# Performance work log

Measured on AMD Instinct MI355X. Metric: run time of the kernel, lower is better.

Reference implementation:

```python
import math
import jax, jax.numpy as jnp
import numpy as np

HIDDEN = 1024
HEADS = 16
HEAD_DIM = 64
THETA = 10000.0
TRAIN_LEN = 2048
SCALE = 4.0
ALPHA = 1.0
BETA = 32.0
B, T = 2, 2048


def _yarn_inv_freq_and_mscale():
    """YaRN (NTK-by-parts) inverse frequencies + attention mscale."""
    half = HEAD_DIM // 2
    pos_freqs = THETA ** (jnp.arange(half, dtype=jnp.float32) * 2.0 / HEAD_DIM)
    inv_freq_extra = 1.0 / pos_freqs              # extrapolation (original RoPE)
    inv_freq_inter = 1.0 / (SCALE * pos_freqs)    # interpolation (position scaling)

    def find_dim(num_rot):
        return (HEAD_DIM * math.log(TRAIN_LEN / (num_rot * 2.0 * math.pi))) / (2.0 * math.log(THETA))

    low = max(math.floor(find_dim(BETA)), 0)
    high = min(math.ceil(find_dim(ALPHA)), half - 1)
    ramp = jnp.clip((jnp.arange(half, dtype=jnp.float32) - low) / max(high - low, 1e-3), 0.0, 1.0)
    extrap_factor = 1.0 - ramp  # 1 -> pure extrapolation (high-freq dims)
    inv_freq = inv_freq_inter * (1.0 - extrap_factor) + inv_freq_extra * extrap_factor
    mscale = 0.1 * math.log(SCALE) + 1.0 if SCALE > 1.0 else 1.0
    return inv_freq, mscale


def _rotate_half(x):
    h = x.shape[-1] // 2
    return jnp.concatenate([-x[..., h:], x[..., :h]], axis=-1)


def _apply_rope(q, k, position_ids):
    inv_freq, mscale = _yarn_inv_freq_and_mscale()
    # angles: (B, L, T, HEAD_DIM//2)
    angles = position_ids.astype(jnp.float32)[..., None] * inv_freq
    cos = jnp.concatenate([jnp.cos(angles)] * 2, axis=-1).astype(q.dtype)
    sin = jnp.concatenate([jnp.sin(angles)] * 2, axis=-1).astype(q.dtype)
    q_rot = q * cos + _rotate_half(q) * sin
    k_rot = k * cos + _rotate_half(k) * sin
    return q_rot, k_rot, mscale


def setup_inputs() -> dict:
    key = jax.random.key(0)
    ks = jax.random.split(key, 7)
    packed_embeddings = jax.random.normal(ks[0], (B, HEADS, T, HIDDEN), dtype=jnp.float32)
    position_ids = jnp.sort(jax.random.randint(ks[1], (B, HEADS, T), 0, T), axis=-1).astype(jnp.int32)
    active_mask = jax.random.randint(ks[2], (B, HEADS, T), 0, 2).astype(jnp.bool_)
    # Xavier-uniform per-head projection params
    lim_in = math.sqrt(6.0 / (HIDDEN + HEAD_DIM))
    q_proj = jax.random.uniform(ks[3], (HEADS, HIDDEN, HEAD_DIM), minval=-lim_in, maxval=lim_in, dtype=jnp.float32)
    k_proj = jax.random.uniform(ks[4], (HEADS, HIDDEN, HEAD_DIM), minval=-lim_in, maxval=lim_in, dtype=jnp.float32)
    v_proj = jax.random.uniform(ks[5], (HEADS, HIDDEN, HEAD_DIM), minval=-lim_in, maxval=lim_in, dtype=jnp.float32)
    o_proj = jax.random.uniform(ks[6], (HEADS, HEAD_DIM, HIDDEN), minval=-lim_in, maxval=lim_in, dtype=jnp.float32)
    return {"packed_embeddings": packed_embeddings, "position_ids": position_ids,
            "active_mask": active_mask, "q_proj": q_proj, "k_proj": k_proj,
            "v_proj": v_proj, "o_proj": o_proj}


def reference(packed_embeddings, position_ids, active_mask, q_proj, k_proj, v_proj, o_proj):
    # per-head projections: (B,L,T,d) x (L,d,u) -> (B,L,T,u)
    q = jnp.einsum('bltd,ldu->bltu', packed_embeddings, q_proj)
    k = jnp.einsum('bltd,ldu->bltu', packed_embeddings, k_proj)
    v = jnp.einsum('bltd,ldu->bltu', packed_embeddings, v_proj)
    q, k, mscale = _apply_rope(q, k, position_ids)

    # cache=None path: num_tokens_processed = 0, key mask = active mask, key_len = T
    scale = mscale / math.sqrt(HEAD_DIM)
    scores = jnp.einsum('bltu,blsu->blts', q, k) * scale  # (B,L,T,T)
    causal = jnp.tril(jnp.ones((T, T), dtype=jnp.bool_))
    mask = active_mask[:, :, :, None] & active_mask[:, :, None, :] & causal
    neg = jnp.finfo(scores.dtype).min
    probs = jax.nn.softmax(jnp.where(mask, scores, neg), axis=-1)
    attended = jnp.einsum('blts,blsu->bltu', probs, v)
    # zero fully-masked (inactive) query rows, matching flex_attention skipping them
    attended = attended * active_mask[..., None].astype(attended.dtype)
    return jnp.einsum('bltu,lud->bltd', attended, o_proj)
```

## Files before the change

kernel.cpp:

```cpp
#include <hip/hip_runtime.h>
#include <hip/hip_bf16.h>
#include <math.h>

typedef __attribute__((ext_vector_type(8))) short bf16x8;
typedef __attribute__((ext_vector_type(4))) float f32x4;

static constexpr int Bn = 2, Ln = 16, Tn = 2048, Dn = 1024, Un = 64;
static constexpr float SCALE_ATTN = 0.14232867951f;
static constexpr int VTS = 2080;

__device__ __forceinline__ unsigned short f2bf(float x) {
    __hip_bfloat16 h = __float2bfloat16(x);
    return *reinterpret_cast<unsigned short*>(&h);
}
__device__ __forceinline__ unsigned int pk2(float a, float b) {
    return (unsigned int)f2bf(a) | ((unsigned int)f2bf(b) << 16);
}
__device__ __forceinline__ float inv_freq_of(int d) {
    float p = powf(10000.0f, (float)d * (1.0f / 32.0f));
    float ramp = fminf(fmaxf(((float)d - 8.0f) * (1.0f / 13.0f), 0.0f), 1.0f);
    return (0.25f / p) * ramp + (1.0f / p) * (1.0f - ramp);
}

__global__ __launch_bounds__(256) void prep_w(
    const float* __restrict__ qp, const float* __restrict__ kp,
    const float* __restrict__ vp, const float* __restrict__ op,
    unsigned short* __restrict__ qt, unsigned short* __restrict__ kt,
    unsigned short* __restrict__ vt, unsigned short* __restrict__ ot)
{
    __shared__ unsigned short T[64][72];
    const int m = blockIdx.z, l = blockIdx.y, x = blockIdx.x;
    const int tid = (int)threadIdx.x;
    const float* sb = (m == 0 ? qp : m == 1 ? kp : m == 2 ? vp : op) + (size_t)l * 65536;
    unsigned short* db = (m == 0 ? qt : m == 1 ? kt : m == 2 ? vt : ot) + (size_t)l * 65536;
    #pragma unroll
    for (int p = 0; p < 4; ++p) {
        int r = (tid >> 4) + 16 * p, c4 = (tid & 15) * 4;
        size_t s = (m < 3) ? ((size_t)(64 * x + r) * 64 + c4)
                           : ((size_t)r * 1024 + 64 * x + c4);
        float4 v = *(const float4*)(sb + s);
        T[r][c4 + 0] = f2bf(v.x); T[r][c4 + 1] = f2bf(v.y);
        T[r][c4 + 2] = f2bf(v.z); T[r][c4 + 3] = f2bf(v.w);
    }
    __syncthreads();
    #pragma unroll
    for (int p = 0; p < 2; ++p) {
        int task = tid + 256 * p;
        int c = task >> 3, g = task & 7;
        uint4 wv; unsigned short* wp = (unsigned short*)&wv;
        #pragma unroll
        for (int j = 0; j < 8; ++j) wp[j] = T[8 * g + j][c];
        size_t d = (m < 3) ? ((size_t)c * 1024 + 64 * x + 8 * g)
                           : ((size_t)(64 * x + c) * 64 + 8 * g);
        *(uint4*)(db + d) = wv;
    }
}

__global__ __launch_bounds__(256) void qkv_rope(
    const float* __restrict__ emb, const int* __restrict__ pos,
    const unsigned short* __restrict__ qt, const unsigned short* __restrict__ kt,
    const unsigned short* __restrict__ vt,
    unsigned short* __restrict__ Qw, unsigned short* __restrict__ Kw,
    unsigned short* __restrict__ Vt)
{
    __shared__ unsigned short A_lds[64][40];
    __shared__ unsigned short O_lds[64][200];
    const int z = blockIdx.y, l = z & 15, row0 = blockIdx.x * 64;
    const int tid = (int)threadIdx.x;
    const int w = tid >> 6, lane = tid & 63, hi = lane >> 4, lo = lane & 15;

    f32x4 acc[12];
    #pragma unroll
    for (int i = 0; i < 12; ++i) acc[i] = (f32x4){0.f, 0.f, 0.f, 0.f};

    const float* embB = emb + ((size_t)z * Tn + row0) * Dn;
    const unsigned short* wq = qt + (size_t)l * 65536;
    const unsigned short* wk = kt + (size_t)l * 65536;
    const unsigned short* wv = vt + (size_t)l * 65536;

    for (int k0 = 0; k0 < Dn; k0 += 32) {
        {
            int r = tid >> 2, c8 = (tid & 3) * 8;
            const float* s = embB + (size_t)r * Dn + k0 + c8;
            float4 v0 = *(const float4*)s, v1 = *(const float4*)(s + 4);
            uint4 u = {pk2(v0.x, v0.y), pk2(v0.z, v0.w), pk2(v1.x, v1.y), pk2(v1.z, v1.w)};
            *(uint4*)&A_lds[r][c8] = u;
        }
        __syncthreads();
        bf16x8 a = *(const bf16x8*)&A_lds[16 * w + lo][8 * hi];
        #pragma unroll
        for (int n = 0; n < 12; ++n) {
            const unsigned short* wb = (n < 4) ? wq : (n < 8) ? wk : wv;
            const unsigned short* bp = wb + (size_t)(16 * (n & 3) + lo) * 1024 + k0 + 8 * hi;
            bf16x8 b = *(const bf16x8*)bp;
            acc[n] = __builtin_amdgcn_mfma_f32_16x16x32_bf16(a, b, acc[n], 0, 0, 0);
        }
        __syncthreads();
    }

    const float if0 = inv_freq_of(lo);
    const float if1 = inv_freq_of(16 + lo);
    #pragma unroll
    for (int r = 0; r < 4; ++r) {
        int orow = 16 * w + 4 * hi + r;
        float fp = (float)pos[(size_t)z * Tn + row0 + orow];
        float s0, c0, s1, c1;
        sincosf(fp * if0, &s0, &c0);
        sincosf(fp * if1, &s1, &c1);
        float qa = acc[0][r], qb = acc[2][r], qc = acc[1][r], qd = acc[3][r];
        O_lds[orow][lo]           = f2bf(qa * c0 - qb * s0);
        O_lds[orow][lo + 32]      = f2bf(qb * c0 + qa * s0);
        O_lds[orow][16 + lo]      = f2bf(qc * c1 - qd * s1);
        O_lds[orow][16 + lo + 32] = f2bf(qd * c1 + qc * s1);
        float ka = acc[4][r], kb = acc[6][r], kc = acc[5][r], kd = acc[7][r];
        O_lds[orow][64 + lo]      = f2bf(ka * c0 - kb * s0);
        O_lds[orow][64 + lo + 32] = f2bf(kb * c0 + ka * s0);
        O_lds[orow][80 + lo]      = f2bf(kc * c1 - kd * s1);
        O_lds[orow][80 + lo + 32] = f2bf(kd * c1 + kc * s1);
        O_lds[orow][128 + lo]     = f2bf(acc[8][r]);
        O_lds[orow][144 + lo]     = f2bf(acc[9][r]);
        O_lds[orow][160 + lo]     = f2bf(acc[10][r]);
        O_lds[orow][176 + lo]     = f2bf(acc[11][r]);
    }
    __syncthreads();
    #pragma unroll
    for (int p = 0; p < 2; ++p) {
        int task = tid + 256 * p, t = task >> 3, g = task & 7;
        *(uint4*)(Qw + ((size_t)z * Tn + row0 + t) * 64 + 8 * g) = *(uint4*)&O_lds[t][8 * g];
        *(uint4*)(Kw + ((size_t)z * Tn + row0 + t) * 64 + 8 * g) = *(uint4*)&O_lds[t][64 + 8 * g];
    }
    #pragma unroll
    for (int p = 0; p < 2; ++p) {
        int task = tid + 256 * p, d = task & 63, g = task >> 6;
        uint4 wv4; unsigned short* wp = (unsigned short*)&wv4;
        #pragma unroll
        for (int j = 0; j < 8; ++j) wp[j] = O_lds[8 * g + j][128 + d];
        *(uint4*)(Vt + (size_t)z * 64 * VTS + (size_t)d * VTS + row0 + 8 * g) = wv4;
    }
}

__global__ __launch_bounds__(256) void flash_attn(
    const unsigned short* __restrict__ Qw, const unsigned short* __restrict__ Kw,
    const unsigned short* __restrict__ Vt, const int* __restrict__ act,
    unsigned short* __restrict__ At)
{
    __shared__ unsigned short K_lds[64][72];
    __shared__ unsigned short V_lds[64][72];
    __shared__ unsigned short P_lds[64][72];
    __shared__ unsigned char aK[64];
    const int z = blockIdx.y;
    const int rt = (int)gridDim.x - 1 - (int)blockIdx.x;
    const int row0 = rt * 64;
    const int tid = (int)threadIdx.x;
    const int w = tid >> 6, lane = tid & 63, hi = lane >> 4, lo = lane & 15;

    const unsigned short* qb = Qw + ((size_t)z * Tn + row0 + 16 * w + lo) * 64 + 8 * hi;
    bf16x8 aq0 = *(const bf16x8*)qb;
    bf16x8 aq1 = *(const bf16x8*)(qb + 32);

    bool aqv[4]; float m_[4], ls[4];
    f32x4 accO[4];
    #pragma unroll
    for (int r = 0; r < 4; ++r) {
        aqv[r] = act[(size_t)z * Tn + row0 + 16 * w + 4 * hi + r] != 0;
        m_[r] = -INFINITY; ls[r] = 0.f;
        accO[r] = (f32x4){0.f, 0.f, 0.f, 0.f};
    }

    for (int kt = 0; kt <= rt; ++kt) {
        const int j0 = kt * 64;
        __syncthreads();
        {
            int r = tid >> 2, c = tid & 3;
            const unsigned short* s = Kw + ((size_t)z * Tn + j0 + r) * 64 + 16 * c;
            *(uint4*)&K_lds[r][16 * c]     = *(const uint4*)s;
            *(uint4*)&K_lds[r][16 * c + 8] = *(const uint4*)(s + 8);
            const unsigned short* v = Vt + (size_t)z * 64 * VTS + (size_t)r * VTS + j0 + 16 * c;
            *(uint4*)&V_lds[r][16 * c]     = *(const uint4*)v;
            *(uint4*)&V_lds[r][16 * c + 8] = *(const uint4*)(v + 8);
        }
        if (tid < 64) aK[tid] = (unsigned char)(act[(size_t)z * Tn + j0 + tid] != 0);
        __syncthreads();

        f32x4 s4[4];
        #pragma unroll
        for (int n = 0; n < 4; ++n) s4[n] = (f32x4){0.f, 0.f, 0.f, 0.f};
        #pragma unroll
        for (int n = 0; n < 4; ++n) {
            bf16x8 b0 = *(const bf16x8*)&K_lds[16 * n + lo][8 * hi];
            bf16x8 b1 = *(const bf16x8*)&K_lds[16 * n + lo][32 + 8 * hi];
            s4[n] = __builtin_amdgcn_mfma_f32_16x16x32_bf16(aq0, b0, s4[n], 0, 0, 0);
            s4[n] = __builtin_amdgcn_mfma_f32_16x16x32_bf16(aq1, b1, s4[n], 0, 0, 0);
        }
        unsigned char akn[4];
        #pragma unroll
        for (int n = 0; n < 4; ++n) akn[n] = aK[16 * n + lo];

        #pragma unroll
        for (int r = 0; r < 4; ++r) {
            const int rowg = row0 + 16 * w + 4 * hi + r;
            float sv[4];
            #pragma unroll
            for (int n = 0; n < 4; ++n) {
                int col = j0 + 16 * n + lo;
                sv[n] = (aqv[r] && akn[n] && col <= rowg) ? s4[n][r] * SCALE_ATTN : -INFINITY;
            }
            float mt = fmaxf(fmaxf(sv[0], sv[1]), fmaxf(sv[2], sv[3]));
            mt = fmaxf(mt, __shfl_xor(mt, 1));
            mt = fmaxf(mt, __shfl_xor(mt, 2));
            mt = fmaxf(mt, __shfl_xor(mt, 4));
            mt = fmaxf(mt, __shfl_xor(mt, 8));
            float mnew = fmaxf(m_[r], mt);
            float p[4], corr;
            if (mnew == -INFINITY) {
                p[0] = p[1] = p[2] = p[3] = 0.f; corr = 1.f;
            } else {
                corr = __expf(m_[r] - mnew);
                #pragma unroll
                for (int n = 0; n < 4; ++n) p[n] = __expf(sv[n] - mnew);
            }
            float ps = p[0] + p[1] + p[2] + p[3];
            ps += __shfl_xor(ps, 1);
            ps += __shfl_xor(ps, 2);
            ps += __shfl_xor(ps, 4);
            ps += __shfl_xor(ps, 8);
            m_[r] = mnew;
            ls[r] = ls[r] * corr + ps;
            #pragma unroll
            for (int n2 = 0; n2 < 4; ++n2) accO[n2][r] *= corr;
            int prow = 16 * w + 4 * hi + r;
            P_lds[prow][lo]      = f2bf(p[0]);
            P_lds[prow][16 + lo] = f2bf(p[1]);
            P_lds[prow][32 + lo] = f2bf(p[2]);
            P_lds[prow][48 + lo] = f2bf(p[3]);
        }
        __syncthreads();

        bf16x8 ap0 = *(const bf16x8*)&P_lds[16 * w + lo][8 * hi];
        bf16x8 ap1 = *(const bf16x8*)&P_lds[16 * w + lo][32 + 8 * hi];
        #pragma unroll
        for (int n2 = 0; n2 < 4; ++n2) {
            bf16x8 b0 = *(const bf16x8*)&V_lds[16 * n2 + lo][8 * hi];
            bf16x8 b1 = *(const bf16x8*)&V_lds[16 * n2 + lo][32 + 8 * hi];
            accO[n2] = __builtin_amdgcn_mfma_f32_16x16x32_bf16(ap0, b0, accO[n2], 0, 0, 0);
            accO[n2] = __builtin_amdgcn_mfma_f32_16x16x32_bf16(ap1, b1, accO[n2], 0, 0, 0);
        }
    }

    #pragma unroll
    for (int r = 0; r < 4; ++r) {
        float inv = (aqv[r] && ls[r] > 0.f) ? 1.0f / ls[r] : 0.f;
        int prow = 16 * w + 4 * hi + r;
        P_lds[prow][lo]      = f2bf(accO[0][r] * inv);
        P_lds[prow][16 + lo] = f2bf(accO[1][r] * inv);
        P_lds[prow][32 + lo] = f2bf(accO[2][r] * inv);
        P_lds[prow][48 + lo] = f2bf(accO[3][r] * inv);
    }
    __syncthreads();
    #pragma unroll
    for (int p = 0; p < 2; ++p) {
        int task = tid + 256 * p, t = task >> 3, g = task & 7;
        *(uint4*)(At + ((size_t)z * Tn + row0 + t) * 64 + 8 * g) = *(uint4*)&P_lds[t][8 * g];
    }
}

__global__ __launch_bounds__(256) void oproj(
    const unsigned short* __restrict__ At, const unsigned short* __restrict__ ot,
    float* __restrict__ out)
{
    __shared__ unsigned short A_lds[64][72];
    const int row0 = (int)blockIdx.y * 64;
    const int c0 = (int)blockIdx.x * 128;
    const int l = (row0 >> 11) & 15;
    const int tid = (int)threadIdx.x;
    const int w = tid >> 6, lane = tid & 63, hi = lane >> 4, lo = lane & 15;
    {
        int r = tid >> 2, c = tid & 3;
        const unsigned short* s = At + ((size_t)row0 + r) * 64 + 16 * c;
        *(uint4*)&A_lds[r][16 * c]     = *(const uint4*)s;
        *(uint4*)&A_lds[r][16 * c + 8] = *(const uint4*)(s + 8);
    }
    __syncthreads();
    bf16x8 a0 = *(const bf16x8*)&A_lds[16 * w + lo][8 * hi];
    bf16x8 a1 = *(const bf16x8*)&A_lds[16 * w + lo][32 + 8 * hi];
    const unsigned short* ob = ot + (size_t)l * 65536;
    f32x4 acc[8];
    #pragma unroll
    for (int n = 0; n < 8; ++n) acc[n] = (f32x4){0.f, 0.f, 0.f, 0.f};
    #pragma unroll
    for (int n = 0; n < 8; ++n) {
        const unsigned short* bp = ob + (size_t)(c0 + 16 * n + lo) * 64;
        bf16x8 b0 = *(const bf16x8*)(bp + 8 * hi);
        bf16x8 b1 = *(const bf16x8*)(bp + 32 + 8 * hi);
        acc[n] = __builtin_amdgcn_mfma_f32_16x16x32_bf16(a0, b0, acc[n], 0, 0, 0);
        acc[n] = __builtin_amdgcn_mfma_f32_16x16x32_bf16(a1, b1, acc[n], 0, 0, 0);
    }
    #pragma unroll
    for (int n = 0; n < 8; ++n)
        #pragma unroll
        for (int r = 0; r < 4; ++r)
            out[(size_t)(row0 + 16 * w + 4 * hi + r) * 1024 + c0 + 16 * n + lo] = acc[n][r];
}

extern "C" void kernel_launch(void* const* d_in, const int* in_sizes, int n_in,
                              void* d_out, int out_size, void* d_ws, size_t ws_size,
                              hipStream_t stream) {
    const float* emb = (const float*)d_in[0];
    const int* pos = (const int*)d_in[1];
    const int* act = (const int*)d_in[2];
    const float* qp = (const float*)d_in[3];
    const float* kp = (const float*)d_in[4];
    const float* vp = (const float*)d_in[5];
    const float* op = (const float*)d_in[6];
    float* out = (float*)d_out;

    unsigned char* W = (unsigned char*)d_ws;
    unsigned short* qt = (unsigned short*)(W + (size_t)0);
    unsigned short* kt = (unsigned short*)(W + ((size_t)2 << 20));
    unsigned short* vt = (unsigned short*)(W + ((size_t)4 << 20));
    unsigned short* ot = (unsigned short*)(W + ((size_t)6 << 20));
    unsigned short* Qw = (unsigned short*)(W + ((size_t)8 << 20));
    unsigned short* Kw = (unsigned short*)(W + ((size_t)16 << 20));
    unsigned short* At = (unsigned short*)(W + ((size_t)24 << 20));
    unsigned short* Vt = (unsigned short*)(W + ((size_t)32 << 20));

    dim3 blk(256);
    prep_w<<<dim3(16, 16, 4), blk, 0, stream>>>(qp, kp, vp, op, qt, kt, vt, ot);
    qkv_rope<<<dim3(Tn / 64, Bn * Ln), blk, 0, stream>>>(emb, pos, qt, kt, vt, Qw, Kw, Vt);
    flash_attn<<<dim3(Tn / 64, Bn * Ln), blk, 0, stream>>>(Qw, Kw, Vt, act, At);
    oproj<<<dim3(Dn / 128, (Bn * Ln * Tn) / 64), blk, 0, stream>>>(At, ot, out);
}
```

Before: 766.7 us.

## Double-buffer QKV projection tiles in LDS with k-chunked weight layout

Weights are pre-transposed into a k-chunked layout (32-wide k slices contiguous per chunk), so each projection step loads weight tiles with coalesced 16-byte reads and stages them in LDS. Embedding and weight tiles are double-buffered: the next chunk's global loads are issued before the MFMAs on the current chunk, hiding load latency. The change adds LDS usage, held in a union with the output staging buffer, plus extra registers for the prefetched data.

```diff
diff --git a/kernel.cpp b/kernel.cpp
--- a/kernel.cpp
+++ b/kernel.cpp
@@ -43,16 +43,28 @@
         T[r][c4 + 2] = f2bf(v.z); T[r][c4 + 3] = f2bf(v.w);
     }
     __syncthreads();
-    #pragma unroll
-    for (int p = 0; p < 2; ++p) {
-        int task = tid + 256 * p;
-        int c = task >> 3, g = task & 7;
-        uint4 wv; unsigned short* wp = (unsigned short*)&wv;
-        #pragma unroll
-        for (int j = 0; j < 8; ++j) wp[j] = T[8 * g + j][c];
-        size_t d = (m < 3) ? ((size_t)c * 1024 + 64 * x + 8 * g)
-                           : ((size_t)(64 * x + c) * 64 + 8 * g);
-        *(uint4*)(db + d) = wv;
+    if (m < 3) {
+        #pragma unroll
+        for (int p = 0; p < 2; ++p) {
+            int task = tid + 256 * p;
+            int u = task >> 3, kio = task & 7;
+            uint4 wv; unsigned short* wp = (unsigned short*)&wv;
+            #pragma unroll
+            for (int j = 0; j < 8; ++j) wp[j] = T[8 * kio + j][u];
+            size_t d = (size_t)(2 * x + (kio >> 2)) * 2048 + (size_t)u * 32 + 8 * (kio & 3);
+            *(uint4*)(db + d) = wv;
+        }
+    } else {
+        #pragma unroll
+        for (int p = 0; p < 2; ++p) {
+            int task = tid + 256 * p;
+            int c = task >> 3, g = task & 7;
+            uint4 wv; unsigned short* wp = (unsigned short*)&wv;
+            #pragma unroll
+            for (int j = 0; j < 8; ++j) wp[j] = T[8 * g + j][c];
+            size_t d = (size_t)(64 * x + c) * 64 + 8 * g;
+            *(uint4*)(db + d) = wv;
+        }
     }
 }
 
@@ -63,8 +75,14 @@
     unsigned short* __restrict__ Qw, unsigned short* __restrict__ Kw,
     unsigned short* __restrict__ Vt)
 {
-    __shared__ unsigned short A_lds[64][40];
-    __shared__ unsigned short O_lds[64][200];
+    __shared__ union {
+        struct {
+            unsigned short A[2][64][40];
+            unsigned short W[2][3][64][40];
+        } st;
+        unsigned short O[64][200];
+    } sm;
+
     const int z = blockIdx.y, l = z & 15, row0 = blockIdx.x * 64;
     const int tid = (int)threadIdx.x;
     const int w = tid >> 6, lane = tid & 63, hi = lane >> 4, lo = lane & 15;
@@ -74,29 +92,48 @@
     for (int i = 0; i < 12; ++i) acc[i] = (f32x4){0.f, 0.f, 0.f, 0.f};
 
     const float* embB = emb + ((size_t)z * Tn + row0) * Dn;
-    const unsigned short* wq = qt + (size_t)l * 65536;
-    const unsigned short* wk = kt + (size_t)l * 65536;
-    const unsigned short* wv = vt + (size_t)l * 65536;
-
-    for (int k0 = 0; k0 < Dn; k0 += 32) {
-        {
-            int r = tid >> 2, c8 = (tid & 3) * 8;
-            const float* s = embB + (size_t)r * Dn + k0 + c8;
-            float4 v0 = *(const float4*)s, v1 = *(const float4*)(s + 4);
-            uint4 u = {pk2(v0.x, v0.y), pk2(v0.z, v0.w), pk2(v1.x, v1.y), pk2(v1.z, v1.w)};
-            *(uint4*)&A_lds[r][c8] = u;
+    const unsigned short* wb[3] = {qt + (size_t)l * 65536, kt + (size_t)l * 65536,
+                                   vt + (size_t)l * 65536};
+
+    float4 pa0, pa1; uint4 pw0, pw1, pw2;
+    const int ar = tid >> 2, ac8 = (tid & 3) * 8;
+    #define LDR(s) do {                                                        \
+        const float* _s = embB + (size_t)ar * Dn + (s) * 32 + ac8;             \
+        pa0 = *(const float4*)_s; pa1 = *(const float4*)(_s + 4);              \
+        size_t _w = (size_t)(s) * 2048 + (size_t)tid * 8;                      \
+        pw0 = *(const uint4*)(wb[0] + _w);                                     \
+        pw1 = *(const uint4*)(wb[1] + _w);                                     \
+        pw2 = *(const uint4*)(wb[2] + _w);                                     \
+    } while (0)
+    #define STR(buf) do {                                                     \
+        uint4 _u = {pk2(pa0.x, pa0.y), pk2(pa0.z, pa0.w),                      \
+                    pk2(pa1.x, pa1.y), pk2(pa1.z, pa1.w)};                     \
+        *(uint4*)&sm.st.A[buf][ar][ac8] = _u;                                  \
+        *(uint4*)&sm.st.W[buf][0][tid >> 2][(tid & 3) * 8] = pw0;              \
+        *(uint4*)&sm.st.W[buf][1][tid >> 2][(tid & 3) * 8] = pw1;              \
+        *(uint4*)&sm.st.W[buf][2][tid >> 2][(tid & 3) * 8] = pw2;              \
+    } while (0)
+
+    LDR(0);
+    STR(0);
+    __syncthreads();
+    for (int s = 0; s < 32; ++s) {
+        const int cur = s & 1;
+        if (s + 1 < 32) LDR(s + 1);
+        bf16x8 a = *(const bf16x8*)&sm.st.A[cur][16 * w + lo][8 * hi];
+        #pragma unroll
+        for (int n = 0; n < 12; ++n) {
+            bf16x8 b = *(const bf16x8*)&sm.st.W[cur][n >> 2][16 * (n & 3) + lo][8 * hi];
+            acc[n] = __builtin_amdgcn_mfma_f32_16x16x32_bf16(a, b, acc[n], 0, 0, 0);
         }
         __syncthreads();
-        bf16x8 a = *(const bf16x8*)&A_lds[16 * w + lo][8 * hi];
-        #pragma unroll
-        for (int n = 0; n < 12; ++n) {
-            const unsigned short* wb = (n < 4) ? wq : (n < 8) ? wk : wv;
-            const unsigned short* bp = wb + (size_t)(16 * (n & 3) + lo) * 1024 + k0 + 8 * hi;
-            bf16x8 b = *(const bf16x8*)bp;
-            acc[n] = __builtin_amdgcn_mfma_f32_16x16x32_bf16(a, b, acc[n], 0, 0, 0);
-        }
-        __syncthreads();
-    }
+        if (s + 1 < 32) {
+            STR(cur ^ 1);
+            __syncthreads();
+        }
+    }
+    #undef LDR
+    #undef STR
 
     const float if0 = inv_freq_of(lo);
     const float if1 = inv_freq_of(16 + lo);
@@ -108,33 +145,33 @@
         sincosf(fp * if0, &s0, &c0);
         sincosf(fp * if1, &s1, &c1);
         float qa = acc[0][r], qb = acc[2][r], qc = acc[1][r], qd = acc[3][r];
-        O_lds[orow][lo]           = f2bf(qa * c0 - qb * s0);
-        O_lds[orow][lo + 32]      = f2bf(qb * c0 + qa * s0);
-        O_lds[orow][16 + lo]      = f2bf(qc * c1 - qd * s1);
-        O_lds[orow][16 + lo + 32] = f2bf(qd * c1 + qc * s1);
+        sm.O[orow][lo]           = f2bf(qa * c0 - qb * s0);
+        sm.O[orow][lo + 32]      = f2bf(qb * c0 + qa * s0);
+        sm.O[orow][16 + lo]      = f2bf(qc * c1 - qd * s1);
+        sm.O[orow][16 + lo + 32] = f2bf(qd * c1 + qc * s1);
         float ka = acc[4][r], kb = acc[6][r], kc = acc[5][r], kd = acc[7][r];
-        O_lds[orow][64 + lo]      = f2bf(ka * c0 - kb * s0);
-        O_lds[orow][64 + lo + 32] = f2bf(kb * c0 + ka * s0);
-        O_lds[orow][80 + lo]      = f2bf(kc * c1 - kd * s1);
-        O_lds[orow][80 + lo + 32] = f2bf(kd * c1 + kc * s1);
-        O_lds[orow][128 + lo]     = f2bf(acc[8][r]);
-        O_lds[orow][144 + lo]     = f2bf(acc[9][r]);
-        O_lds[orow][160 + lo]     = f2bf(acc[10][r]);
-        O_lds[orow][176 + lo]     = f2bf(acc[11][r]);
+        sm.O[orow][64 + lo]      = f2bf(ka * c0 - kb * s0);
+        sm.O[orow][64 + lo + 32] = f2bf(kb * c0 + ka * s0);
+        sm.O[orow][80 + lo]      = f2bf(kc * c1 - kd * s1);
+        sm.O[orow][80 + lo + 32] = f2bf(kd * c1 + kc * s1);
+        sm.O[orow][128 + lo]     = f2bf(acc[8][r]);
+        sm.O[orow][144 + lo]     = f2bf(acc[9][r]);
+        sm.O[orow][160 + lo]     = f2bf(acc[10][r]);
+        sm.O[orow][176 + lo]     = f2bf(acc[11][r]);
     }
     __syncthreads();
     #pragma unroll
     for (int p = 0; p < 2; ++p) {
         int task = tid + 256 * p, t = task >> 3, g = task & 7;
-        *(uint4*)(Qw + ((size_t)z * Tn + row0 + t) * 64 + 8 * g) = *(uint4*)&O_lds[t][8 * g];
-        *(uint4*)(Kw + ((size_t)z * Tn + row0 + t) * 64 + 8 * g) = *(uint4*)&O_lds[t][64 + 8 * g];
+        *(uint4*)(Qw + ((size_t)z * Tn + row0 + t) * 64 + 8 * g) = *(uint4*)&sm.O[t][8 * g];
+        *(uint4*)(Kw + ((size_t)z * Tn + row0 + t) * 64 + 8 * g) = *(uint4*)&sm.O[t][64 + 8 * g];
     }
     #pragma unroll
     for (int p = 0; p < 2; ++p) {
         int task = tid + 256 * p, d = task & 63, g = task >> 6;
         uint4 wv4; unsigned short* wp = (unsigned short*)&wv4;
         #pragma unroll
-        for (int j = 0; j < 8; ++j) wp[j] = O_lds[8 * g + j][128 + d];
+        for (int j = 0; j < 8; ++j) wp[j] = sm.O[8 * g + j][128 + d];
         *(uint4*)(Vt + (size_t)z * 64 * VTS + (size_t)d * VTS + row0 + 8 * g) = wv4;
     }
 }
```

New measurement: 682.6 us. -11.0%, faster.
